# Optimization experiments

Hardware: AMD Instinct MI355X
Metric: run time of the kernel (lower is better)

## Reference

```python
import jax, jax.numpy as jnp
import numpy as np

N_NODES = 100000
N_EDGES = 1600000
D = 128
H = 256
EPS = 1e-5


def _bn(x, gamma, beta):
    # BatchNorm1d in training mode: biased batch statistics
    mu = x.mean(axis=0)
    var = jnp.mean((x - mu) ** 2, axis=0)
    return (x - mu) * jax.lax.rsqrt(var + EPS) * gamma + beta


def setup_inputs() -> dict:
    key = jax.random.key(0)
    ks = jax.random.split(key, 6)
    inp = {
        "input": jax.random.normal(ks[0], (N_NODES, D), dtype=jnp.float32),
        "adj_rows": jax.random.randint(ks[1], (N_EDGES,), 0, N_NODES, dtype=jnp.int32),
        "adj_cols": jax.random.randint(ks[2], (N_EDGES,), 0, N_NODES, dtype=jnp.int32),
        "adj_vals": jax.random.uniform(ks[3], (N_EDGES,), dtype=jnp.float32),
        "gamma1": jnp.ones((2 * D,), jnp.float32),
        "beta1": jnp.zeros((2 * D,), jnp.float32),
        "W1": jax.random.normal(ks[4], (2 * D, H), dtype=jnp.float32) * (1.0 / np.sqrt(2 * D)),
        "b1": jnp.zeros((H,), jnp.float32),
        "gamma2": jnp.ones((H,), jnp.float32),
        "beta2": jnp.zeros((H,), jnp.float32),
        "W2": jax.random.normal(ks[5], (H, D), dtype=jnp.float32) * (1.0 / np.sqrt(H)),
        "b2": jnp.zeros((D,), jnp.float32),
    }
    return inp


def reference(input, adj_rows, adj_cols, adj_vals, gamma1, beta1, W1, b1, gamma2, beta2, W2, b2):
    n = input.shape[0]
    # phi is identity; spmm(adj, x): gather source features, weight, scatter-add by row
    messages = adj_vals[:, None] * input[adj_cols]          # [E, D]
    aggregated = jax.ops.segment_sum(messages, adj_rows, num_segments=n)  # [n, D]
    # agg == 'cat'
    x = jnp.concatenate([input, aggregated], axis=1)        # [n, 2D]
    # MLP: BN -> Linear -> BN -> ReLU -> Linear (dropout p=0)
    x = _bn(x, gamma1, beta1)
    x = x @ W1 + b1
    x = _bn(x, gamma2, beta2)
    x = jax.nn.relu(x)
    x = x @ W2 + b2
    return x
```

## Files before the change

### kernel.cpp

```cpp
#include <hip/hip_runtime.h>

#define N_D 128
#define N_H 256
#define EPSV 1e-5f
#define STAT_ROWS 256
#define NS1 16
#define NS2 32
#define NB 1024
#define PERB 2304
#define CPAD 16

typedef unsigned short u16;
typedef __attribute__((ext_vector_type(8))) short short8;
typedef __attribute__((ext_vector_type(4))) float floatx4;

__device__ __forceinline__ float bf2f(unsigned u) {
    return __uint_as_float(u << 16);
}
__device__ __forceinline__ u16 f2bf(float f) {
    unsigned u = __float_as_uint(f);
    return (u16)((u + 0x7FFFu + ((u >> 16) & 1u)) >> 16);
}

__global__ __launch_bounds__(256) void convin_kernel(
    const float* __restrict__ input, u16* __restrict__ xbf, int n)
{
    int gid = blockIdx.x * 256 + threadIdx.x;
    if (gid < n * 32) {
        int r = gid >> 5, c4 = (gid & 31) * 4;
        float4 v = *(const float4*)&input[(size_t)r * N_D + c4];
        unsigned p0 = f2bf(v.x) | ((unsigned)f2bf(v.y) << 16);
        unsigned p1 = f2bf(v.z) | ((unsigned)f2bf(v.w) << 16);
        *(uint2*)&xbf[(size_t)r * 256 + c4] = make_uint2(p0, p1);
    }
}

__global__ __launch_bounds__(1024) void bucket_kernel(
    const int* __restrict__ rows, const int* __restrict__ cols,
    const float* __restrict__ vals, int* __restrict__ cursor,
    int2* __restrict__ staged, int E, unsigned inv_pr, int per_rows)
{
    __shared__ int hist[NB];
    __shared__ int base[NB];
    __shared__ int lcnt[NB];
    int t = threadIdx.x;
    hist[t] = 0;
    __syncthreads();
    int per = (E + (int)gridDim.x - 1) / (int)gridDim.x;
    int lo = blockIdx.x * per;
    int hi = min(E, lo + per);
    for (int e = lo + t; e < hi; e += 1024) {
        int b = (int)__umulhi((unsigned)rows[e], inv_pr);
        atomicAdd(&hist[b], 1);
    }
    __syncthreads();
    {
        int h = hist[t];
        base[t] = h ? atomicAdd(&cursor[t * CPAD], h) : 0;
        lcnt[t] = 0;
    }
    __syncthreads();
    for (int e = lo + t; e < hi; e += 1024) {
        int r = rows[e];
        int b = (int)__umulhi((unsigned)r, inv_pr);
        int rl = r - b * per_rows;
        int idx = base[b] + atomicAdd(&lcnt[b], 1);
        if (idx < PERB)
            staged[(size_t)b * PERB + idx] =
                make_int2(cols[e] | (rl << 17), __float_as_int(vals[e]));
    }
}

__global__ __launch_bounds__(1024) void scan_buckets_kernel(
    const int* __restrict__ cursor, int* __restrict__ bucketBase)
{
    __shared__ int sm[NB];
    int t = threadIdx.x;
    int v = min(cursor[t * CPAD], PERB);
    sm[t] = v;
    __syncthreads();
    for (int off = 1; off < NB; off <<= 1) {
        int x = (t >= off) ? sm[t - off] : 0;
        __syncthreads();
        sm[t] += x;
        __syncthreads();
    }
    bucketBase[t] = sm[t] - v;
}

__global__ __launch_bounds__(256) void place_kernel(
    const int* __restrict__ cursor, const int* __restrict__ bucketBase,
    const int2* __restrict__ staged, int2* __restrict__ edges,
    int* __restrict__ rowPtr, int* __restrict__ cnt, int n, int per_rows)
{
    __shared__ int hist[128];
    __shared__ int scn[128];
    __shared__ int lcnt[128];
    int b = blockIdx.x;
    int t = threadIdx.x;
    int r0 = b * per_rows;
    if (r0 >= n) return;
    if (t < 128) { hist[t] = 0; lcnt[t] = 0; }
    __syncthreads();
    int count = min(cursor[b * CPAD], PERB);
    const int2* sb = staged + (size_t)b * PERB;
    for (int i = t; i < count; i += 256)
        atomicAdd(&hist[((unsigned)sb[i].x) >> 17], 1);
    __syncthreads();
    if (t < 128) scn[t] = hist[t];
    __syncthreads();
    for (int off = 1; off < 128; off <<= 1) {
        int x = (t < 128 && t >= off) ? scn[t - off] : 0;
        __syncthreads();
        if (t < 128) scn[t] += x;
        __syncthreads();
    }
    int base = bucketBase[b];
    if (t < per_rows && r0 + t < n) {
        rowPtr[r0 + t] = base + scn[t] - hist[t];
        cnt[r0 + t] = hist[t];
    }
    __syncthreads();
    for (int i = t; i < count; i += 256) {
        int2 en = sb[i];
        int rl = ((unsigned)en.x) >> 17;
        int idx = atomicAdd(&lcnt[rl], 1);
        edges[base + scn[rl] - hist[rl] + idx] = make_int2(en.x & 0x1FFFF, en.y);
    }
}

__global__ __launch_bounds__(256) void aggregate_kernel(
    const unsigned* __restrict__ xin,
    const int* __restrict__ rowPtr, const int* __restrict__ cnt,
    const int2* __restrict__ edges,
    unsigned* __restrict__ xout, int n)
{
    int wave = (blockIdx.x * 256 + threadIdx.x) >> 6;
    if (wave >= n) return;
    int lane = threadIdx.x & 63;
    int half = lane >> 5;
    int ll = lane & 31;
    const uint2* xin2 = (const uint2*)xin;
    int e = rowPtr[wave];
    int end = e + cnt[wave];
    float4 a0 = {0.f,0.f,0.f,0.f}, a1 = {0.f,0.f,0.f,0.f};
    float4 a2 = {0.f,0.f,0.f,0.f}, a3 = {0.f,0.f,0.f,0.f};

#define ACC4(acc, pp, vv) { \
        acc.x += (vv) * bf2f((pp).x & 0xFFFF); \
        acc.y += (vv) * bf2f((pp).x >> 16); \
        acc.z += (vv) * bf2f((pp).y & 0xFFFF); \
        acc.w += (vv) * bf2f((pp).y >> 16); }

    if ((e & 1) && e < end) {
        int2 ed = edges[e];
        float v = half ? 0.f : __int_as_float(ed.y);
        uint2 p = xin2[(size_t)ed.x * 64 + ll];
        ACC4(a0, p, v);
        ++e;
    }
    for (; e + 7 < end; e += 8) {
        int4 q0 = *(const int4*)&edges[e];
        int4 q1 = *(const int4*)&edges[e + 2];
        int4 q2 = *(const int4*)&edges[e + 4];
        int4 q3 = *(const int4*)&edges[e + 6];
        int   c0 = half ? q0.z : q0.x;
        int   c1 = half ? q1.z : q1.x;
        int   c2 = half ? q2.z : q2.x;
        int   c3 = half ? q3.z : q3.x;
        float v0 = __int_as_float(half ? q0.w : q0.y);
        float v1 = __int_as_float(half ? q1.w : q1.y);
        float v2 = __int_as_float(half ? q2.w : q2.y);
        float v3 = __int_as_float(half ? q3.w : q3.y);
        uint2 p0 = xin2[(size_t)c0 * 64 + ll];
        uint2 p1 = xin2[(size_t)c1 * 64 + ll];
        uint2 p2 = xin2[(size_t)c2 * 64 + ll];
        uint2 p3 = xin2[(size_t)c3 * 64 + ll];
        ACC4(a0, p0, v0);
        ACC4(a1, p1, v1);
        ACC4(a2, p2, v2);
        ACC4(a3, p3, v3);
    }
    for (; e + 1 < end; e += 2) {
        int4 q0 = *(const int4*)&edges[e];
        int   c0 = half ? q0.z : q0.x;
        float v0 = __int_as_float(half ? q0.w : q0.y);
        uint2 p0 = xin2[(size_t)c0 * 64 + ll];
        ACC4(a0, p0, v0);
    }
    if (e < end) {
        int2 ed = edges[e];
        float v = half ? 0.f : __int_as_float(ed.y);
        uint2 p = xin2[(size_t)ed.x * 64 + ll];
        ACC4(a0, p, v);
    }
#undef ACC4

    a0.x += a1.x + a2.x + a3.x;
    a0.y += a1.y + a2.y + a3.y;
    a0.z += a1.z + a2.z + a3.z;
    a0.w += a1.w + a2.w + a3.w;
    float bx = __shfl(a0.x, ll + 32, 64);
    float by = __shfl(a0.y, ll + 32, 64);
    float bz = __shfl(a0.z, ll + 32, 64);
    float bw = __shfl(a0.w, ll + 32, 64);
    if (half == 0) {
        a0.x += bx; a0.y += by; a0.z += bz; a0.w += bw;
        uint2 pk;
        pk.x = f2bf(a0.x) | ((unsigned)f2bf(a0.y) << 16);
        pk.y = f2bf(a0.z) | ((unsigned)f2bf(a0.w) << 16);
        ((uint2*)xout)[(size_t)wave * 64 + 32 + ll] = pk;
    }
}

__global__ __launch_bounds__(256) void xstats_kernel(
    const u16* __restrict__ xbf, float* __restrict__ s1s, int n)
{
    int t = threadIdx.x;
    int r0 = blockIdx.x * STAT_ROWS;
    int r1 = min(n, r0 + STAT_ROWS);
    float s = 0.f, q = 0.f;
    for (int r = r0; r < r1; ++r) {
        float x = bf2f((unsigned)xbf[(size_t)r * 256 + t]);
        s += x; q += x * x;
    }
    float* base = s1s + (size_t)(blockIdx.x & (NS1 - 1)) * 512;
    atomicAdd(&base[t], s);
    atomicAdd(&base[256 + t], q);
}

__global__ __launch_bounds__(256) void prep1a_kernel(
    const float* __restrict__ s1s,
    const float* __restrict__ gamma1, const float* __restrict__ beta1,
    float* __restrict__ a1, float* __restrict__ c1, float n)
{
    int t = threadIdx.x;
    float sum = 0.f, sq = 0.f;
#pragma unroll
    for (int s = 0; s < NS1; ++s) {
        sum += s1s[s * 512 + t];
        sq  += s1s[s * 512 + 256 + t];
    }
    float mu = sum / n;
    float var = sq / n - mu * mu;
    float rs = rsqrtf(var + EPSV);
    float a = rs * gamma1[t];
    a1[t] = a;
    c1[t] = beta1[t] - mu * a;
}

__global__ __launch_bounds__(256) void convw1_kernel(
    const float* __restrict__ W1, const float* __restrict__ a1,
    const float* __restrict__ c1, const float* __restrict__ b1,
    u16* __restrict__ W1bt, float* __restrict__ b1p)
{
    __shared__ float red[256];
    int nIdx = blockIdx.x;
    int k = threadIdx.x;
    float w = W1[(size_t)k * N_H + nIdx];
    W1bt[(size_t)nIdx * 256 + k] = f2bf(a1[k] * w);
    red[k] = c1[k] * w;
    __syncthreads();
    for (int s = 128; s > 0; s >>= 1) {
        if (k < s) red[k] += red[k + s];
        __syncthreads();
    }
    if (k == 0) b1p[nIdx] = red[0] + b1[nIdx];
}

__global__ __launch_bounds__(256) void convw2_kernel(
    const float* __restrict__ W2, u16* __restrict__ W2bt)
{
    int nIdx = blockIdx.x;
    int k = threadIdx.x;
    W2bt[(size_t)nIdx * 256 + k] = f2bf(W2[(size_t)k * N_D + nIdx]);
}

__global__ __launch_bounds__(256) void prep2_kernel(
    const float* __restrict__ s2s,
    const float* __restrict__ gamma2, const float* __restrict__ beta2,
    float* __restrict__ a2, float* __restrict__ c2, float n)
{
    int t = threadIdx.x;
    float sum = 0.f, sq = 0.f;
#pragma unroll
    for (int s = 0; s < NS2; ++s) {
        sum += s2s[s * 512 + t];
        sq  += s2s[s * 512 + 256 + t];
    }
    float mu = sum / n;
    float var = sq / n - mu * mu;
    float rs = rsqrtf(var + EPSV);
    float a = rs * gamma2[t];
    a2[t] = a;
    c2[t] = beta2[t] - mu * a;
}

__global__ __launch_bounds__(256, 3) void gemm1_kernel(
    const u16* __restrict__ xbf, const u16* __restrict__ W1bt,
    const float* __restrict__ b1p, u16* __restrict__ ybf,
    float* __restrict__ s2s, int n)
{
    __shared__ __align__(16) u16 T[64 * 136];
    __shared__ float ssum[128];
    __shared__ float ssq[128];
    int t = threadIdx.x;
    int w = t >> 6, l = t & 63;
    int row0 = blockIdx.x * 64;
    int col0 = blockIdx.y * 128;
    int wrow = (w & 1) * 32, wcol = (w >> 1) * 64;
    int lm = l & 15, lq = l >> 4;
    if (t < 128) { ssum[t] = 0.f; ssq[t] = 0.f; }

    floatx4 acc[2][4];
#pragma unroll
    for (int i = 0; i < 2; ++i)
#pragma unroll
        for (int j = 0; j < 4; ++j) acc[i][j] = (floatx4){0.f, 0.f, 0.f, 0.f};

    const u16* Ab = xbf + (size_t)(row0 + wrow + lm) * 256 + lq * 8;
    const u16* Bb = W1bt + (size_t)(col0 + wcol + lm) * 256 + lq * 8;

#pragma unroll
    for (int h = 0; h < 2; ++h) {
        const int kh = h * 128;
        short8 aR[4][2], bR[4][4];
#pragma unroll
        for (int s = 0; s < 4; ++s) {
            int k = kh + s * 32;
            aR[s][0] = *(const short8*)&Ab[k];
            aR[s][1] = *(const short8*)&Ab[4096 + k];
            bR[s][0] = *(const short8*)&Bb[k];
            bR[s][1] = *(const short8*)&Bb[4096 + k];
            bR[s][2] = *(const short8*)&Bb[8192 + k];
            bR[s][3] = *(const short8*)&Bb[12288 + k];
        }
#pragma unroll
        for (int s = 0; s < 4; ++s)
#pragma unroll
            for (int fm = 0; fm < 2; ++fm)
#pragma unroll
                for (int fn = 0; fn < 4; ++fn)
                    acc[fm][fn] = __builtin_amdgcn_mfma_f32_16x16x32_bf16(
                        aR[s][fm], bR[s][fn], acc[fm][fn], 0, 0, 0);
    }

    __syncthreads();
    float cs[4] = {0.f, 0.f, 0.f, 0.f};
    float cq[4] = {0.f, 0.f, 0.f, 0.f};
#pragma unroll
    for (int fn = 0; fn < 4; ++fn) {
        int cl = wcol + fn * 16 + lm;
        float bb = b1p[col0 + cl];
#pragma unroll
        for (int fm = 0; fm < 2; ++fm) {
            int rl = wrow + fm * 16 + lq * 4;
#pragma unroll
            for (int i = 0; i < 4; ++i) {
                float v = acc[fm][fn][i] + bb;
                T[(rl + i) * 136 + cl] = f2bf(v);
                if (row0 + rl + i < n) { cs[fn] += v; cq[fn] += v * v; }
            }
        }
        atomicAdd(&ssum[cl], cs[fn]);
        atomicAdd(&ssq[cl], cq[fn]);
    }
    __syncthreads();
    float* sbase = s2s + (size_t)(blockIdx.x & (NS2 - 1)) * 512;
    if (t < 128) {
        atomicAdd(&sbase[col0 + t], ssum[t]);
        atomicAdd(&sbase[256 + col0 + t], ssq[t]);
    }
#pragma unroll
    for (int p = 0; p < 4; ++p) {
        int r = p * 16 + (t >> 4);
        if (row0 + r < n)
            *(uint4*)&ybf[(size_t)(row0 + r) * 256 + col0 + (t & 15) * 8] =
                *(const uint4*)&T[r * 136 + (t & 15) * 8];
    }
}

__device__ __forceinline__ short8 bn_relu_pack(
    uint4 raw, float4 aa0, float4 aa1, float4 cc0, float4 cc1)
{
    float z0 = fmaxf(bf2f(raw.x & 0xFFFF) * aa0.x + cc0.x, 0.f);
    float z1 = fmaxf(bf2f(raw.x >> 16)    * aa0.y + cc0.y, 0.f);
    float z2 = fmaxf(bf2f(raw.y & 0xFFFF) * aa0.z + cc0.z, 0.f);
    float z3 = fmaxf(bf2f(raw.y >> 16)    * aa0.w + cc0.w, 0.f);
    float z4 = fmaxf(bf2f(raw.z & 0xFFFF) * aa1.x + cc1.x, 0.f);
    float z5 = fmaxf(bf2f(raw.z >> 16)    * aa1.y + cc1.y, 0.f);
    float z6 = fmaxf(bf2f(raw.w & 0xFFFF) * aa1.z + cc1.z, 0.f);
    float z7 = fmaxf(bf2f(raw.w >> 16)    * aa1.w + cc1.w, 0.f);
    uint4 pk;
    pk.x = f2bf(z0) | ((unsigned)f2bf(z1) << 16);
    pk.y = f2bf(z2) | ((unsigned)f2bf(z3) << 16);
    pk.z = f2bf(z4) | ((unsigned)f2bf(z5) << 16);
    pk.w = f2bf(z6) | ((unsigned)f2bf(z7) << 16);
    return *(short8*)&pk;
}

__global__ __launch_bounds__(256, 2) void gemm2_kernel(
    const u16* __restrict__ ybf, const u16* __restrict__ W2bt,
    const float* __restrict__ a2, const float* __restrict__ c2,
    const float* __restrict__ b2, float* __restrict__ out, int n)
{
    int t = threadIdx.x;
    int w = t >> 6, l = t & 63;
    int row0 = blockIdx.x * 64;
    int wrow = (w & 1) * 32, wcol = (w >> 1) * 64;
    int lm = l & 15, lq = l >> 4;

    floatx4 acc[2][4];
#pragma unroll
    for (int i = 0; i < 2; ++i)
#pragma unroll
        for (int j = 0; j < 4; ++j) acc[i][j] = (floatx4){0.f, 0.f, 0.f, 0.f};

    const u16* Ab = ybf + (size_t)(row0 + wrow + lm) * 256 + lq * 8;
    const u16* Bb = W2bt + (size_t)(wcol + lm) * 256 + lq * 8;
    int kbase = lq * 8;

#pragma unroll
    for (int h = 0; h < 2; ++h) {
        const int kh = h * 128;
        uint4 yR[4][2];
        short8 bR[4][4];
#pragma unroll
        for (int s = 0; s < 4; ++s) {
            int k = kh + s * 32;
            yR[s][0] = *(const uint4*)&Ab[k];
            yR[s][1] = *(const uint4*)&Ab[4096 + k];
            bR[s][0] = *(const short8*)&Bb[k];
            bR[s][1] = *(const short8*)&Bb[4096 + k];
            bR[s][2] = *(const short8*)&Bb[8192 + k];
            bR[s][3] = *(const short8*)&Bb[12288 + k];
        }
#pragma unroll
        for (int s = 0; s < 4; ++s) {
            int kc = kh + s * 32 + kbase;
            float4 aa0 = *(const float4*)&a2[kc];
            float4 aa1 = *(const float4*)&a2[kc + 4];
            float4 cc0 = *(const float4*)&c2[kc];
            float4 cc1 = *(const float4*)&c2[kc + 4];
            short8 af0 = bn_relu_pack(yR[s][0], aa0, aa1, cc0, cc1);
            short8 af1 = bn_relu_pack(yR[s][1], aa0, aa1, cc0, cc1);
#pragma unroll
            for (int fn = 0; fn < 4; ++fn) {
                acc[0][fn] = __builtin_amdgcn_mfma_f32_16x16x32_bf16(
                    af0, bR[s][fn], acc[0][fn], 0, 0, 0);
                acc[1][fn] = __builtin_amdgcn_mfma_f32_16x16x32_bf16(
                    af1, bR[s][fn], acc[1][fn], 0, 0, 0);
            }
        }
    }

#pragma unroll
    for (int fn = 0; fn < 4; ++fn) {
        int c = wcol + fn * 16 + lm;
        float bb = b2[c];
#pragma unroll
        for (int fm = 0; fm < 2; ++fm) {
            int rbase = row0 + wrow + fm * 16 + lq * 4;
#pragma unroll
            for (int i = 0; i < 4; ++i) {
                int r = rbase + i;
                if (r < n) out[(size_t)r * N_D + c] = acc[fm][fn][i] + bb;
            }
        }
    }
}

extern "C" void kernel_launch(void* const* d_in, const int* in_sizes, int n_in,
                              void* d_out, int out_size, void* d_ws, size_t ws_size,
                              hipStream_t stream)
{
    const float* input    = (const float*)d_in[0];
    const int*   adj_rows = (const int*)d_in[1];
    const int*   adj_cols = (const int*)d_in[2];
    const float* adj_vals = (const float*)d_in[3];
    const float* gamma1   = (const float*)d_in[4];
    const float* beta1    = (const float*)d_in[5];
    const float* W1       = (const float*)d_in[6];
    const float* b1       = (const float*)d_in[7];
    const float* gamma2   = (const float*)d_in[8];
    const float* beta2    = (const float*)d_in[9];
    const float* W2       = (const float*)d_in[10];
    const float* b2       = (const float*)d_in[11];

    int n = in_sizes[0] / N_D;
    int E = in_sizes[1];
    size_t n_pad = ((size_t)n + 127) & ~(size_t)127;

    u16* xbf = (u16*)d_ws;
    u16* ybf = xbf + n_pad * 256;
    int2* edges = (int2*)ybf;
    int2* staged = edges + E;
    u16* W1bt = ybf + n_pad * 256;
    u16* W2bt = W1bt + 256 * 256;
    float* stats  = (float*)(W2bt + 128 * 256);
    float* a1     = stats;
    float* c1     = stats + 256;
    float* b1p    = stats + 512;
    float* a2     = stats + 768;
    float* c2     = stats + 1024;
    float* s1s    = stats + 1280;
    float* s2s    = s1s + NS1 * 512;
    int* cursor     = (int*)(s2s + NS2 * 512);
    int* bucketBase = cursor + NB * CPAD;
    int* rowPtr     = bucketBase + NB;
    int* cnt        = rowPtr + n;

    hipMemsetAsync(cursor, 0, (size_t)NB * CPAD * sizeof(int), stream);
    hipMemsetAsync(s1s, 0, (size_t)(NS1 + NS2) * 512 * sizeof(float), stream);

    convin_kernel<<<(n * 32 + 255) / 256, 256, 0, stream>>>(input, xbf, n);
    convw2_kernel<<<128, 256, 0, stream>>>(W2, W2bt);

    int per_rows = (n + NB - 1) / NB;
    unsigned inv_pr = (unsigned)((((unsigned long long)1 << 32) + per_rows - 1) / per_rows);

    bucket_kernel<<<256, 1024, 0, stream>>>(
        adj_rows, adj_cols, adj_vals, cursor, staged, E, inv_pr, per_rows);
    scan_buckets_kernel<<<1, 1024, 0, stream>>>(cursor, bucketBase);
    place_kernel<<<NB, 256, 0, stream>>>(
        cursor, bucketBase, staged, edges, rowPtr, cnt, n, per_rows);

    aggregate_kernel<<<(n + 3) / 4, 256, 0, stream>>>(
        (const unsigned*)xbf, rowPtr, cnt, edges, (unsigned*)xbf, n);

    xstats_kernel<<<(n + STAT_ROWS - 1) / STAT_ROWS, 256, 0, stream>>>(xbf, s1s, n);

    prep1a_kernel<<<1, 256, 0, stream>>>(s1s, gamma1, beta1, a1, c1, (float)n);
    convw1_kernel<<<256, 256, 0, stream>>>(W1, a1, c1, b1, W1bt, b1p);

    dim3 g1((unsigned)(n_pad / 64), 2);
    gemm1_kernel<<<g1, 256, 0, stream>>>(xbf, W1bt, b1p, ybf, s2s, n);

    prep2_kernel<<<1, 256, 0, stream>>>(s2s, gamma2, beta2, a2, c2, (float)n);

    gemm2_kernel<<<(unsigned)(n_pad / 64), 256, 0, stream>>>(ybf, W2bt, a2, c2, b2, (float*)d_out, n);
}
```

Baseline: 472.7 us.

## Stage GEMM A/B tiles into swizzled LDS via direct global-to-LDS loads

Both GEMM kernels now stage the 64-row activation tile and weight slices into XOR-swizzled shared memory, using global_load_lds for raw copies. Each block then loops over output column chunks, so the A tile is read from global once instead of once per column-block. gemm1 drops the 2-D grid, and gemm2 applies BN+ReLU once while staging. Outputs are written through swizzled LDS for coalesced stores. The cost is larger LDS use, which lowers occupancy, plus extra barriers and serialised weight restaging between chunks.

```diff
diff --git a/kernel.cpp b/kernel.cpp
--- a/kernel.cpp
+++ b/kernel.cpp
@@ -20,6 +20,13 @@
 __device__ __forceinline__ u16 f2bf(float f) {
     unsigned u = __float_as_uint(f);
     return (u16)((u + 0x7FFFu + ((u >> 16) & 1u)) >> 16);
+}
+__device__ __forceinline__ void load16_to_lds(const void* g, void* l) {
+    auto gp = reinterpret_cast<const unsigned int __attribute__((address_space(1)))*>(
+        reinterpret_cast<uintptr_t>(g));
+    auto lp = reinterpret_cast<unsigned int __attribute__((address_space(3)))*>(
+        reinterpret_cast<uintptr_t>(l));
+    __builtin_amdgcn_global_load_lds(gp, lp, 16, 0, 0);
 }
 
 __global__ __launch_bounds__(256) void convin_kernel(
@@ -296,87 +303,105 @@
     c2[t] = beta2[t] - mu * a;
 }
 
-__global__ __launch_bounds__(256, 3) void gemm1_kernel(
+
+__device__ __forceinline__ int swzA(int row, int c16) {
+    return (row << 8) + (((c16) ^ (row & 15)) << 3);
+}
+
+__device__ __forceinline__ void stage_swz(
+    const u16* __restrict__ g, u16* lds, int t, int nu4)
+{
+    for (int base = 0; base < nu4; base += 256) {
+        int idx = base + t;
+        int row = idx >> 5;
+        int c16 = (idx & 31) ^ (row & 15);
+        load16_to_lds(g + (size_t)row * 256 + c16 * 8,
+                      &lds[(size_t)(base + (t & 192)) * 8]);
+    }
+}
+
+__global__ __launch_bounds__(256, 2) void gemm1_kernel(
     const u16* __restrict__ xbf, const u16* __restrict__ W1bt,
     const float* __restrict__ b1p, u16* __restrict__ ybf,
     float* __restrict__ s2s, int n)
 {
-    __shared__ __align__(16) u16 T[64 * 136];
-    __shared__ float ssum[128];
-    __shared__ float ssq[128];
+    __shared__ __align__(16) u16 As[64 * 256];
+    __shared__ __align__(16) u16 Bs[64 * 256];
+    __shared__ __align__(16) u16 T[64 * 64];
+    __shared__ float ssum[64];
+    __shared__ float ssq[64];
     int t = threadIdx.x;
     int w = t >> 6, l = t & 63;
     int row0 = blockIdx.x * 64;
-    int col0 = blockIdx.y * 128;
-    int wrow = (w & 1) * 32, wcol = (w >> 1) * 64;
+    int wrow = (w & 1) * 32, wcol = (w >> 1) * 32;
     int lm = l & 15, lq = l >> 4;
-    if (t < 128) { ssum[t] = 0.f; ssq[t] = 0.f; }
-
-    floatx4 acc[2][4];
-#pragma unroll
-    for (int i = 0; i < 2; ++i)
-#pragma unroll
-        for (int j = 0; j < 4; ++j) acc[i][j] = (floatx4){0.f, 0.f, 0.f, 0.f};
-
-    const u16* Ab = xbf + (size_t)(row0 + wrow + lm) * 256 + lq * 8;
-    const u16* Bb = W1bt + (size_t)(col0 + wcol + lm) * 256 + lq * 8;
-
-#pragma unroll
-    for (int h = 0; h < 2; ++h) {
-        const int kh = h * 128;
-        short8 aR[4][2], bR[4][4];
-#pragma unroll
-        for (int s = 0; s < 4; ++s) {
-            int k = kh + s * 32;
-            aR[s][0] = *(const short8*)&Ab[k];
-            aR[s][1] = *(const short8*)&Ab[4096 + k];
-            bR[s][0] = *(const short8*)&Bb[k];
-            bR[s][1] = *(const short8*)&Bb[4096 + k];
-            bR[s][2] = *(const short8*)&Bb[8192 + k];
-            bR[s][3] = *(const short8*)&Bb[12288 + k];
-        }
-#pragma unroll
-        for (int s = 0; s < 4; ++s)
+
+    stage_swz(xbf + (size_t)row0 * 256, As, t, 2048);
+    stage_swz(W1bt, Bs, t, 2048);
+    if (t < 64) { ssum[t] = 0.f; ssq[t] = 0.f; }
+    __syncthreads();
+
+    for (int c = 0; c < 4; ++c) {
+        int col0g = c * 64;
+        floatx4 acc[2][2];
+#pragma unroll
+        for (int i = 0; i < 2; ++i)
+#pragma unroll
+            for (int j = 0; j < 2; ++j) acc[i][j] = (floatx4){0.f,0.f,0.f,0.f};
+#pragma unroll
+        for (int ks = 0; ks < 8; ++ks) {
+            short8 af[2], bfr[2];
+#pragma unroll
+            for (int f = 0; f < 2; ++f) {
+                int ar = wrow + f * 16 + lm;
+                af[f]  = *(const short8*)&As[swzA(ar, ks * 4 + lq)];
+                int br = wcol + f * 16 + lm;
+                bfr[f] = *(const short8*)&Bs[swzA(br, ks * 4 + lq)];
+            }
 #pragma unroll
             for (int fm = 0; fm < 2; ++fm)
 #pragma unroll
-                for (int fn = 0; fn < 4; ++fn)
+                for (int fn = 0; fn < 2; ++fn)
                     acc[fm][fn] = __builtin_amdgcn_mfma_f32_16x16x32_bf16(
-                        aR[s][fm], bR[s][fn], acc[fm][fn], 0, 0, 0);
-    }
-
-    __syncthreads();
-    float cs[4] = {0.f, 0.f, 0.f, 0.f};
-    float cq[4] = {0.f, 0.f, 0.f, 0.f};
-#pragma unroll
-    for (int fn = 0; fn < 4; ++fn) {
-        int cl = wcol + fn * 16 + lm;
-        float bb = b1p[col0 + cl];
-#pragma unroll
-        for (int fm = 0; fm < 2; ++fm) {
-            int rl = wrow + fm * 16 + lq * 4;
-#pragma unroll
-            for (int i = 0; i < 4; ++i) {
-                float v = acc[fm][fn][i] + bb;
-                T[(rl + i) * 136 + cl] = f2bf(v);
-                if (row0 + rl + i < n) { cs[fn] += v; cq[fn] += v * v; }
+                        af[fm], bfr[fn], acc[fm][fn], 0, 0, 0);
+        }
+#pragma unroll
+        for (int fn = 0; fn < 2; ++fn) {
+            int cl = wcol + fn * 16 + lm;
+            float bb = b1p[col0g + cl];
+            float cs = 0.f, cq = 0.f;
+#pragma unroll
+            for (int fm = 0; fm < 2; ++fm) {
+                int rl = wrow + fm * 16 + lq * 4;
+#pragma unroll
+                for (int i = 0; i < 4; ++i) {
+                    float v = acc[fm][fn][i] + bb;
+                    int r = rl + i;
+                    T[(r << 6) + ((((cl >> 3) ^ (r & 7)) << 3) | (cl & 7))] = f2bf(v);
+                    if (row0 + r < n) { cs += v; cq += v * v; }
+                }
             }
-        }
-        atomicAdd(&ssum[cl], cs[fn]);
-        atomicAdd(&ssq[cl], cq[fn]);
-    }
-    __syncthreads();
-    float* sbase = s2s + (size_t)(blockIdx.x & (NS2 - 1)) * 512;
-    if (t < 128) {
-        atomicAdd(&sbase[col0 + t], ssum[t]);
-        atomicAdd(&sbase[256 + col0 + t], ssq[t]);
-    }
-#pragma unroll
-    for (int p = 0; p < 4; ++p) {
-        int r = p * 16 + (t >> 4);
-        if (row0 + r < n)
-            *(uint4*)&ybf[(size_t)(row0 + r) * 256 + col0 + (t & 15) * 8] =
-                *(const uint4*)&T[r * 136 + (t & 15) * 8];
+            atomicAdd(&ssum[cl], cs);
+            atomicAdd(&ssq[cl], cq);
+        }
+        __syncthreads();
+#pragma unroll
+        for (int p = 0; p < 2; ++p) {
+            int r = p * 32 + (t >> 3);
+            int s = t & 7;
+            if (row0 + r < n)
+                *(uint4*)&ybf[(size_t)(row0 + r) * 256 + col0g + s * 8] =
+                    *(const uint4*)&T[(r << 6) + ((s ^ (r & 7)) << 3)];
+        }
+        float* sbase = s2s + (size_t)(blockIdx.x & (NS2 - 1)) * 512;
+        if (t < 64) {
+            atomicAdd(&sbase[col0g + t], ssum[t]);
+            atomicAdd(&sbase[256 + col0g + t], ssq[t]);
+            ssum[t] = 0.f; ssq[t] = 0.f;
+        }
+        if (c < 3)
+            stage_swz(W1bt + (size_t)(c + 1) * 64 * 256, Bs, t, 2048);
+        __syncthreads();
     }
 }
 
@@ -404,69 +429,80 @@
     const float* __restrict__ a2, const float* __restrict__ c2,
     const float* __restrict__ b2, float* __restrict__ out, int n)
 {
+    __shared__ __align__(16) u16 As[64 * 256];
+    __shared__ __align__(16) u16 Bs[32 * 256];
+    __shared__ __align__(16) float Tf[64 * 32];
     int t = threadIdx.x;
     int w = t >> 6, l = t & 63;
     int row0 = blockIdx.x * 64;
-    int wrow = (w & 1) * 32, wcol = (w >> 1) * 64;
+    int wrow = (w & 1) * 32, wcol16 = (w >> 1) * 16;
     int lm = l & 15, lq = l >> 4;
 
-    floatx4 acc[2][4];
-#pragma unroll
-    for (int i = 0; i < 2; ++i)
-#pragma unroll
-        for (int j = 0; j < 4; ++j) acc[i][j] = (floatx4){0.f, 0.f, 0.f, 0.f};
-
-    const u16* Ab = ybf + (size_t)(row0 + wrow + lm) * 256 + lq * 8;
-    const u16* Bb = W2bt + (size_t)(wcol + lm) * 256 + lq * 8;
-    int kbase = lq * 8;
-
-#pragma unroll
-    for (int h = 0; h < 2; ++h) {
-        const int kh = h * 128;
-        uint4 yR[4][2];
-        short8 bR[4][4];
-#pragma unroll
-        for (int s = 0; s < 4; ++s) {
-            int k = kh + s * 32;
-            yR[s][0] = *(const uint4*)&Ab[k];
-            yR[s][1] = *(const uint4*)&Ab[4096 + k];
-            bR[s][0] = *(const short8*)&Bb[k];
-            bR[s][1] = *(const short8*)&Bb[4096 + k];
-            bR[s][2] = *(const short8*)&Bb[8192 + k];
-            bR[s][3] = *(const short8*)&Bb[12288 + k];
-        }
-#pragma unroll
-        for (int s = 0; s < 4; ++s) {
-            int kc = kh + s * 32 + kbase;
-            float4 aa0 = *(const float4*)&a2[kc];
-            float4 aa1 = *(const float4*)&a2[kc + 4];
-            float4 cc0 = *(const float4*)&c2[kc];
-            float4 cc1 = *(const float4*)&c2[kc + 4];
-            short8 af0 = bn_relu_pack(yR[s][0], aa0, aa1, cc0, cc1);
-            short8 af1 = bn_relu_pack(yR[s][1], aa0, aa1, cc0, cc1);
-#pragma unroll
-            for (int fn = 0; fn < 4; ++fn) {
-                acc[0][fn] = __builtin_amdgcn_mfma_f32_16x16x32_bf16(
-                    af0, bR[s][fn], acc[0][fn], 0, 0, 0);
-                acc[1][fn] = __builtin_amdgcn_mfma_f32_16x16x32_bf16(
-                    af1, bR[s][fn], acc[1][fn], 0, 0, 0);
+    {
+        const uint4* src = (const uint4*)(ybf + (size_t)row0 * 256);
+#pragma unroll
+        for (int p = 0; p < 8; ++p) {
+            int idx = p * 256 + t;
+            int row = idx >> 5;
+            int c16 = idx & 31;
+            uint4 raw = src[idx];
+            float4 aa0 = *(const float4*)&a2[c16 * 8];
+            float4 aa1 = *(const float4*)&a2[c16 * 8 + 4];
+            float4 cc0 = *(const float4*)&c2[c16 * 8];
+            float4 cc1 = *(const float4*)&c2[c16 * 8 + 4];
+            short8 z = bn_relu_pack(raw, aa0, aa1, cc0, cc1);
+            *(short8*)&As[swzA(row, c16)] = z;
+        }
+    }
+    stage_swz(W2bt, Bs, t, 1024);
+    __syncthreads();
+
+    for (int c = 0; c < 4; ++c) {
+        int col0g = c * 32;
+        floatx4 acc[2];
+        acc[0] = (floatx4){0.f,0.f,0.f,0.f};
+        acc[1] = (floatx4){0.f,0.f,0.f,0.f};
+#pragma unroll
+        for (int ks = 0; ks < 8; ++ks) {
+            short8 af[2], bfr;
+#pragma unroll
+            for (int f = 0; f < 2; ++f) {
+                int ar = wrow + f * 16 + lm;
+                af[f] = *(const short8*)&As[swzA(ar, ks * 4 + lq)];
             }
-        }
-    }
-
-#pragma unroll
-    for (int fn = 0; fn < 4; ++fn) {
-        int c = wcol + fn * 16 + lm;
-        float bb = b2[c];
-#pragma unroll
-        for (int fm = 0; fm < 2; ++fm) {
-            int rbase = row0 + wrow + fm * 16 + lq * 4;
-#pragma unroll
-            for (int i = 0; i < 4; ++i) {
-                int r = rbase + i;
-                if (r < n) out[(size_t)r * N_D + c] = acc[fm][fn][i] + bb;
+            int br = wcol16 + lm;
+            bfr = *(const short8*)&Bs[swzA(br, ks * 4 + lq)];
+#pragma unroll
+            for (int fm = 0; fm < 2; ++fm)
+                acc[fm] = __builtin_amdgcn_mfma_f32_16x16x32_bf16(
+                    af[fm], bfr, acc[fm], 0, 0, 0);
+        }
+        {
+            int cl = wcol16 + lm;
+            float bb = b2[col0g + cl];
+#pragma unroll
+            for (int fm = 0; fm < 2; ++fm) {
+                int rl = wrow + fm * 16 + lq * 4;
+#pragma unroll
+                for (int i = 0; i < 4; ++i) {
+                    int r = rl + i;
+                    Tf[(r << 5) + ((((cl >> 2) ^ (r & 7)) << 2) | (cl & 3))] =
+                        acc[fm][i] + bb;
+                }
             }
         }
+        __syncthreads();
+#pragma unroll
+        for (int p = 0; p < 2; ++p) {
+            int r = p * 32 + (t >> 3);
+            int s = t & 7;
+            if (row0 + r < n)
+                *(float4*)&out[(size_t)(row0 + r) * N_D + col0g + s * 4] =
+                    *(const float4*)&Tf[(r << 5) + ((s ^ (r & 7)) << 2)];
+        }
+        if (c < 3)
+            stage_swz(W2bt + (size_t)(c + 1) * 32 * 256, Bs, t, 1024);
+        __syncthreads();
     }
 }
 
@@ -533,8 +569,7 @@
     prep1a_kernel<<<1, 256, 0, stream>>>(s1s, gamma1, beta1, a1, c1, (float)n);
     convw1_kernel<<<256, 256, 0, stream>>>(W1, a1, c1, b1, W1bt, b1p);
 
-    dim3 g1((unsigned)(n_pad / 64), 2);
-    gemm1_kernel<<<g1, 256, 0, stream>>>(xbf, W1bt, b1p, ybf, s2s, n);
+    gemm1_kernel<<<(unsigned)(n_pad / 64), 256, 0, stream>>>(xbf, W1bt, b1p, ybf, s2s, n);
 
     prep2_kernel<<<1, 256, 0, stream>>>(s2s, gamma2, beta2, a2, c2, (float)n);
 
```

Result: faster. 426.1 us (-9.9%).
